# Performance work log

Measured on AMD Instinct MI355X. Metric: run time of the kernel, lower is better.

The kernel has to match this reference:

```python
import jax, jax.numpy as jnp
import numpy as np

# sparsity config (from constant.args.sparsity.activation)
N_SP, M_SP = 2, 4      # first-level n:m (keep n of every m channels)
N2_SP, M2_SP = 1, 8    # second-level n2:m2 applied to the residual


def _nm_mask(xa, n, m):
    """Per-block top-n mask over channel blocks of size m.
    xa: non-negative magnitudes, shape (N, C, H, W).
    Keeps entries >= the n-th largest value in each block (ties kept,
    matching torch's `b < topk_val` -> 0 semantics)."""
    N, C, H, W = xa.shape
    b = xa.reshape(N, C // m, m, H, W)
    # n-th largest == ascending-sorted index (m - n); keep dim for broadcast
    thr = jnp.sort(b, axis=2)[:, :, m - n : m - n + 1]
    return (b >= thr).reshape(N, C, H, W)


def setup_inputs() -> dict:
    key = jax.random.key(0)
    x = jax.random.normal(key, (64, 256, 56, 56), dtype=jnp.float32)
    return {"x": x}


def reference(x):
    xa = jnp.abs(x)
    mask1 = _nm_mask(xa, N_SP, M_SP)
    # second-level mask: zero out already-kept entries, then top-n2 of m2 blocks
    resid = jnp.where(mask1, jnp.zeros((), xa.dtype), xa)
    mask2 = _nm_mask(resid, N2_SP, M2_SP)
    mask = mask1 | mask2  # torch does mask += mask2 then .bool()
    return x * mask.astype(x.dtype)
```

## Files before the change

### kernel.cpp

```cpp
#include <hip/hip_runtime.h>


#define N_IMG   64
#define C_CH    256
#define HW      3136
#define HW4     784
#define CH_OCT  32

typedef float vfloat4 __attribute__((ext_vector_type(4)));

__device__ __forceinline__ float second_largest4(float a, float b, float c, float d) {
    float mab = fmaxf(a, b), nab = fminf(a, b);
    float mcd = fmaxf(c, d), ncd = fminf(c, d);
    return fmaxf(fminf(mab, mcd), fmaxf(nab, ncd));
}

__global__ __launch_bounds__(256) void sparsity_kernel(const float* __restrict__ x,
                                                       float* __restrict__ out) {
    const int idx = blockIdx.x * 256 + threadIdx.x;
    const int cb  = blockIdx.y;
    const int n   = idx / HW4;
    const int hw4 = idx - n * HW4;

    const size_t base = (size_t)n * (C_CH * HW) + (size_t)cb * (8 * HW) + (size_t)hw4 * 4;
    const vfloat4* __restrict__ px = (const vfloat4*)(x + base);
    vfloat4* po = (vfloat4*)(out + base);

    vfloat4 v[8];
    #pragma unroll
    for (int c = 0; c < 8; ++c) {
        v[c] = px[c * (HW / 4)];
    }

    #pragma unroll
    for (int e = 0; e < 4; ++e) {
        float a[8];
        #pragma unroll
        for (int c = 0; c < 8; ++c) a[c] = fabsf(v[c][e]);

        const float thr1a = second_largest4(a[0], a[1], a[2], a[3]);
        const float thr1b = second_largest4(a[4], a[5], a[6], a[7]);

        float res[8];
        bool  m1[8];
        #pragma unroll
        for (int c = 0; c < 4; ++c) { m1[c] = a[c] >= thr1a; res[c] = m1[c] ? 0.0f : a[c]; }
        #pragma unroll
        for (int c = 4; c < 8; ++c) { m1[c] = a[c] >= thr1b; res[c] = m1[c] ? 0.0f : a[c]; }

        float thr2 = res[0];
        #pragma unroll
        for (int c = 1; c < 8; ++c) thr2 = fmaxf(thr2, res[c]);

        #pragma unroll
        for (int c = 0; c < 8; ++c) {
            const bool keep = m1[c] | (res[c] >= thr2);
            v[c][e] = keep ? v[c][e] : 0.0f;
        }
    }

    #pragma unroll
    for (int c = 0; c < 8; ++c) {
        po[c * (HW / 4)] = v[c];
    }
}

extern "C" void kernel_launch(void* const* d_in, const int* in_sizes, int n_in,
                              void* d_out, int out_size, void* d_ws, size_t ws_size,
                              hipStream_t stream) {
    const float* x = (const float*)d_in[0];
    float* out = (float*)d_out;
    dim3 grid((N_IMG * HW4) / 256, CH_OCT);
    sparsity_kernel<<<grid, 256, 0, stream>>>(x, out);
}
```

Before: 343.7 us.

## Stage channel-octet slabs through LDS with nontemporal loads and stores

Each 512-thread block now covers one half of an 8-channel slab for one image. It loads the slab into padded shared memory with linear nontemporal loads, applies the mask with 392 threads, then writes the results back through shared memory with nontemporal stores. The goal is more contiguous global access and less cache pollution for a pure streaming kernel. In exchange it adds two barriers, leaves threads idle during the compute phase, and shared-memory use may limit occupancy.

```diff
diff --git a/kernel.cpp b/kernel.cpp
--- a/kernel.cpp
+++ b/kernel.cpp
@@ -1,11 +1,15 @@
 #include <hip/hip_runtime.h>
 
 
-#define N_IMG   64
-#define C_CH    256
-#define HW      3136
-#define HW4     784
-#define CH_OCT  32
+#define N_IMG     64
+#define C_CH      256
+#define HW        3136
+#define HW4       784
+#define CH_OCT    32
+#define HALF_F4   392
+#define LDS_STR   393
+#define SLAB_F4   (8 * HALF_F4)
+#define BLK       512
 
 typedef float vfloat4 __attribute__((ext_vector_type(4)));
 
@@ -15,23 +19,7 @@
     return fmaxf(fminf(mab, mcd), fmaxf(nab, ncd));
 }
 
-__global__ __launch_bounds__(256) void sparsity_kernel(const float* __restrict__ x,
-                                                       float* __restrict__ out) {
-    const int idx = blockIdx.x * 256 + threadIdx.x;
-    const int cb  = blockIdx.y;
-    const int n   = idx / HW4;
-    const int hw4 = idx - n * HW4;
-
-    const size_t base = (size_t)n * (C_CH * HW) + (size_t)cb * (8 * HW) + (size_t)hw4 * 4;
-    const vfloat4* __restrict__ px = (const vfloat4*)(x + base);
-    vfloat4* po = (vfloat4*)(out + base);
-
-    vfloat4 v[8];
-    #pragma unroll
-    for (int c = 0; c < 8; ++c) {
-        v[c] = px[c * (HW / 4)];
-    }
-
+__device__ __forceinline__ void mask_oct(vfloat4 v[8]) {
     #pragma unroll
     for (int e = 0; e < 4; ++e) {
         float a[8];
@@ -58,10 +46,53 @@
             v[c][e] = keep ? v[c][e] : 0.0f;
         }
     }
+}
+
+__global__ __launch_bounds__(BLK) void sparsity_kernel(const float* __restrict__ x,
+                                                       float* __restrict__ out) {
+    __shared__ vfloat4 slab[8 * LDS_STR];
+
+    const int h  = blockIdx.x & 1;
+    const int cb = blockIdx.x >> 1;
+    const int n  = blockIdx.y;
+    const int t  = threadIdx.x;
+
+    const size_t gbase = (size_t)n * (C_CH * HW4) + (size_t)cb * (8 * HW4)
+                       + (size_t)h * HALF_F4;
+    const vfloat4* gx = (const vfloat4*)x + gbase;
+    vfloat4*       go = (vfloat4*)out + gbase;
 
     #pragma unroll
-    for (int c = 0; c < 8; ++c) {
-        po[c * (HW / 4)] = v[c];
+    for (int j = 0; j < 7; ++j) {
+        const int f = j * BLK + t;
+        if (f < SLAB_F4) {
+            const int c   = f / HALF_F4;
+            const int col = f - c * HALF_F4;
+            slab[c * LDS_STR + col] =
+                __builtin_nontemporal_load(&gx[(size_t)c * HW4 + col]);
+        }
+    }
+    __syncthreads();
+
+    if (t < HALF_F4) {
+        vfloat4 v[8];
+        #pragma unroll
+        for (int c = 0; c < 8; ++c) v[c] = slab[c * LDS_STR + t];
+        mask_oct(v);
+        #pragma unroll
+        for (int c = 0; c < 8; ++c) slab[c * LDS_STR + t] = v[c];
+    }
+    __syncthreads();
+
+    #pragma unroll
+    for (int j = 0; j < 7; ++j) {
+        const int f = j * BLK + t;
+        if (f < SLAB_F4) {
+            const int c   = f / HALF_F4;
+            const int col = f - c * HALF_F4;
+            __builtin_nontemporal_store(slab[c * LDS_STR + col],
+                                        &go[(size_t)c * HW4 + col]);
+        }
     }
 }
 
@@ -70,6 +101,6 @@
                               hipStream_t stream) {
     const float* x = (const float*)d_in[0];
     float* out = (float*)d_out;
-    dim3 grid((N_IMG * HW4) / 256, CH_OCT);
-    sparsity_kernel<<<grid, 256, 0, stream>>>(x, out);
+    dim3 grid(2 * CH_OCT, N_IMG);
+    sparsity_kernel<<<grid, BLK, 0, stream>>>(x, out);
 }
```

New measurement: 328.4 us. -4.5%, faster.
